# Kernel tuning notes

Measured on AMD Instinct MI355X. Metric: run time of the kernel, lower is better.

## Reference

```python
import jax, jax.numpy as jnp
import numpy as np

EMBED = 1024
HEADS = 16
HEAD_DIM = EMBED // HEADS
N, S = 2, 2048


def setup_inputs() -> dict:
    key = jax.random.key(0)
    ks = jax.random.split(key, 8)
    scale_p = 1.0 / np.sqrt(HEAD_DIM)
    return {
        "queries": jax.random.normal(ks[0], (N, S, EMBED), jnp.float32),
        "keys": jax.random.normal(ks[1], (N, S, EMBED), jnp.float32),
        "values": jax.random.normal(ks[2], (N, S, EMBED), jnp.float32),
        # per-head projection weights, torch Linear convention: y = x @ W.T
        "Wq": jax.random.normal(ks[3], (HEAD_DIM, HEAD_DIM), jnp.float32) * scale_p,
        "Wk": jax.random.normal(ks[4], (HEAD_DIM, HEAD_DIM), jnp.float32) * scale_p,
        "Wv": jax.random.normal(ks[5], (HEAD_DIM, HEAD_DIM), jnp.float32) * scale_p,
        "Wo": jax.random.normal(ks[6], (EMBED, EMBED), jnp.float32) * (1.0 / np.sqrt(EMBED)),
        "bo": jax.random.normal(ks[7], (EMBED,), jnp.float32) * 0.01,
    }


def reference(queries, keys, values, Wq, Wk, Wv, Wo, bo):
    n, sq, e = queries.shape
    sk = keys.shape[1]
    # split heads: (N, S, H, D)
    q = queries.reshape(n, sq, HEADS, HEAD_DIM)
    k = keys.reshape(n, sk, HEADS, HEAD_DIM)
    v = values.reshape(n, sk, HEADS, HEAD_DIM)
    # per-head linear projections (weights shared across heads), torch Linear: x @ W.T
    q = jnp.einsum('nshd,ed->nshe', q, Wq)
    k = jnp.einsum('nshd,ed->nshe', k, Wk)
    v = jnp.einsum('nshd,ed->nshe', v, Wv)
    # attention scores (N, H, Q, K); NOTE: scaled by sqrt(embed_size), as in source
    energy = jnp.einsum('nqhd,nkhd->nhqk', q, k)
    attention = jax.nn.softmax(energy / jnp.sqrt(jnp.float32(EMBED)), axis=3)
    out = jnp.einsum('nhql,nlhd->nqhd', attention, v).reshape(n, sq, EMBED)
    return out @ Wo.T + bo
```

## Files before the change

kernel.cpp:

```cpp
#include <hip/hip_runtime.h>
#include <hip/hip_bf16.h>

#define NB 2
#define SS 2048
#define EE 1024
#define HH 16
#define DD 64
#define NHD (NB*HH)
#define KT 64

#define QSCALE 0.04508422002777998f

typedef _Float16 half8 __attribute__((ext_vector_type(8)));
typedef _Float16 half4 __attribute__((ext_vector_type(4)));
typedef float floatx4 __attribute__((ext_vector_type(4)));

__device__ __forceinline__ half8 cvt8(const float* p) {
    float4 x = *(const float4*)p;
    float4 y = *(const float4*)(p + 4);
    half8 h = { (_Float16)x.x, (_Float16)x.y, (_Float16)x.z, (_Float16)x.w,
                (_Float16)y.x, (_Float16)y.y, (_Float16)y.z, (_Float16)y.w };
    return h;
}

__device__ __forceinline__ unsigned int pkrtz_u32(float a, float b) {
    return __builtin_bit_cast(unsigned int, __builtin_amdgcn_cvt_pkrtz(a, b));
}

__device__ __forceinline__ int swz64(int row, int colh) {
    return (row << 6) + ((((colh >> 3) ^ (row & 7)) << 3) | (colh & 7));
}

__global__ __launch_bounds__(256) void proj_kernel(
    const float* __restrict__ Q, const float* __restrict__ K, const float* __restrict__ V,
    const float* __restrict__ Wq, const float* __restrict__ Wk, const float* __restrict__ Wv,
    const float* __restrict__ Wo,
    _Float16* __restrict__ Qp, _Float16* __restrict__ Kp, _Float16* __restrict__ Vt,
    _Float16* __restrict__ Wf)
{
    int t = threadIdx.x, lane = t & 63, wid = t >> 6;
    int lr = lane & 15, lg = lane >> 4;
    int b = blockIdx.x;
    int nh = b >> 5, st = b & 31;
    int n = nh >> 4, h = nh & 15;

    if (t < 128) {
        int i = b * 1024 + t * 8;
        *(half8*)(Wf + i) = cvt8(Wo + i);
    }

    __shared__ __align__(16) _Float16 vt[DD][72];

    const size_t xoff = ((size_t)n * SS + st * 64 + wid * 16 + lr) * EE
                        + (size_t)h * DD + lg * 8;
    const size_t qob = ((size_t)nh * SS + st * 64 + wid * 16 + lg * 4) * DD;

    const float* tens[3] = {Q, K, V};
    const float* wts[3]  = {Wq, Wk, Wv};

    #pragma unroll
    for (int x = 0; x < 3; ++x) {
        const float* Xr = tens[x] + xoff;
        half8 a0 = cvt8(Xr);
        half8 a1 = cvt8(Xr + 32);
        floatx4 acc[4];
        #pragma unroll
        for (int ns = 0; ns < 4; ++ns) {
            const float* Wr = wts[x] + (size_t)(ns * 16 + lr) * DD + lg * 8;
            half8 b0 = cvt8(Wr);
            half8 b1 = cvt8(Wr + 32);
            floatx4 c = (floatx4){0.f, 0.f, 0.f, 0.f};
            c = __builtin_amdgcn_mfma_f32_16x16x32_f16(a0, b0, c, 0, 0, 0);
            c = __builtin_amdgcn_mfma_f32_16x16x32_f16(a1, b1, c, 0, 0, 0);
            acc[ns] = c;
        }
        if (x == 0) {
            #pragma unroll
            for (int ns = 0; ns < 4; ++ns)
                #pragma unroll
                for (int r = 0; r < 4; ++r)
                    Qp[qob + (size_t)r * DD + ns * 16 + lr] = (_Float16)(acc[ns][r] * QSCALE);
        } else if (x == 1) {
            #pragma unroll
            for (int ns = 0; ns < 4; ++ns)
                #pragma unroll
                for (int r = 0; r < 4; ++r)
                    Kp[qob + (size_t)r * DD + ns * 16 + lr] = (_Float16)acc[ns][r];
        } else {
            #pragma unroll
            for (int ns = 0; ns < 4; ++ns)
                #pragma unroll
                for (int r = 0; r < 4; ++r)
                    vt[ns * 16 + lr][wid * 16 + lg * 4 + r] = (_Float16)acc[ns][r];
        }
    }
    __syncthreads();
    {
        int d = t >> 2, q4 = (t & 3) * 16;
        _Float16* dst = Vt + ((size_t)nh * DD + d) * SS + st * 64 + q4;
        *(half8*)dst       = *(const half8*)(&vt[d][q4]);
        *(half8*)(dst + 8) = *(const half8*)(&vt[d][q4 + 8]);
    }
}

__global__ __launch_bounds__(256, 4) void attn_kernel(
    const _Float16* __restrict__ Qp, const _Float16* __restrict__ Kp,
    const _Float16* __restrict__ Vt, _Float16* __restrict__ Of)
{
    int b = blockIdx.x;
    int slot = b >> 3;
    int nh = (b & 7) * 4 + (slot & 3);
    int qt = slot >> 2;
    int n = nh >> 4, h = nh & 15;
    int t = threadIdx.x;
    int lane = t & 63, wid = t >> 6;
    int lr = lane & 15;
    int lg = lane >> 4;

    __shared__ __align__(16) _Float16 kbuf[2][KT * DD];
    __shared__ __align__(16) _Float16 vbuf[2][DD * KT];
    __shared__ __align__(16) _Float16 plds[4][16 * 64];

    const _Float16* Qb = Qp + ((size_t)nh * SS + qt * 64 + wid * 16) * DD;
    const _Float16* Kb = Kp + (size_t)nh * SS * DD;
    const _Float16* Vb = Vt + (size_t)nh * DD * SS;

    half8 qf0 = *(const half8*)(Qb + (size_t)lr * DD + lg * 8);
    half8 qf1 = *(const half8*)(Qb + (size_t)lr * DD + 32 + lg * 8);

    half8 ones = { (_Float16)1.f, (_Float16)1.f, (_Float16)1.f, (_Float16)1.f,
                   (_Float16)1.f, (_Float16)1.f, (_Float16)1.f, (_Float16)1.f };

    int sr = t >> 3, sc = (t & 7) * 8;

    {
        half8 k0 = *(const half8*)(Kb + (size_t)sr * DD + sc);
        half8 k1 = *(const half8*)(Kb + (size_t)(sr + 32) * DD + sc);
        half8 v0 = *(const half8*)(Vb + (size_t)sr * SS + sc);
        half8 v1 = *(const half8*)(Vb + (size_t)(sr + 32) * SS + sc);
        *(half8*)(&kbuf[0][swz64(sr, sc)]) = k0;
        *(half8*)(&kbuf[0][swz64(sr + 32, sc)]) = k1;
        *(half8*)(&vbuf[0][swz64(sr, sc)]) = v0;
        *(half8*)(&vbuf[0][swz64(sr + 32, sc)]) = v1;
    }
    __syncthreads();

    floatx4 oacc[4];
    #pragma unroll
    for (int ns = 0; ns < 4; ++ns) oacc[ns] = (floatx4){0.f, 0.f, 0.f, 0.f};
    floatx4 sacc = (floatx4){0.f, 0.f, 0.f, 0.f};

    int p = 0;
    for (int kb = 0; kb < SS; kb += KT, p ^= 1) {
        int kn = (kb + KT) & (SS - 1);
        half8 sk0 = *(const half8*)(Kb + (size_t)(kn + sr) * DD + sc);
        half8 sk1 = *(const half8*)(Kb + (size_t)(kn + sr + 32) * DD + sc);
        half8 sv0 = *(const half8*)(Vb + (size_t)sr * SS + kn + sc);
        half8 sv1 = *(const half8*)(Vb + (size_t)(sr + 32) * SS + kn + sc);

        half8 kf[4][2];
        #pragma unroll
        for (int ns = 0; ns < 4; ++ns) {
            kf[ns][0] = *(const half8*)(&kbuf[p][swz64(ns * 16 + lr, lg * 8)]);
            kf[ns][1] = *(const half8*)(&kbuf[p][swz64(ns * 16 + lr, 32 + lg * 8)]);
        }
        floatx4 s0 = (floatx4){0.f, 0.f, 0.f, 0.f};
        floatx4 s1 = (floatx4){0.f, 0.f, 0.f, 0.f};
        s0 = __builtin_amdgcn_mfma_f32_16x16x32_f16(kf[0][0], qf0, s0, 0, 0, 0);
        s0 = __builtin_amdgcn_mfma_f32_16x16x32_f16(kf[0][1], qf1, s0, 0, 0, 0);
        s1 = __builtin_amdgcn_mfma_f32_16x16x32_f16(kf[1][0], qf0, s1, 0, 0, 0);
        s1 = __builtin_amdgcn_mfma_f32_16x16x32_f16(kf[1][1], qf1, s1, 0, 0, 0);

        {
            float p0 = exp2f(fminf(s0[0], 50.f)), p1 = exp2f(fminf(s0[1], 50.f));
            float p2 = exp2f(fminf(s0[2], 50.f)), p3 = exp2f(fminf(s0[3], 50.f));
            uint2 pr; pr.x = pkrtz_u32(p0, p1); pr.y = pkrtz_u32(p2, p3);
            *(uint2*)(&plds[wid][swz64(lr, 0 * 16 + lg * 4)]) = pr;
        }
        {
            float p0 = exp2f(fminf(s1[0], 50.f)), p1 = exp2f(fminf(s1[1], 50.f));
            float p2 = exp2f(fminf(s1[2], 50.f)), p3 = exp2f(fminf(s1[3], 50.f));
            uint2 pr; pr.x = pkrtz_u32(p0, p1); pr.y = pkrtz_u32(p2, p3);
            *(uint2*)(&plds[wid][swz64(lr, 1 * 16 + lg * 4)]) = pr;
        }

        floatx4 s2 = (floatx4){0.f, 0.f, 0.f, 0.f};
        floatx4 s3 = (floatx4){0.f, 0.f, 0.f, 0.f};
        s2 = __builtin_amdgcn_mfma_f32_16x16x32_f16(kf[2][0], qf0, s2, 0, 0, 0);
        s2 = __builtin_amdgcn_mfma_f32_16x16x32_f16(kf[2][1], qf1, s2, 0, 0, 0);
        s3 = __builtin_amdgcn_mfma_f32_16x16x32_f16(kf[3][0], qf0, s3, 0, 0, 0);
        s3 = __builtin_amdgcn_mfma_f32_16x16x32_f16(kf[3][1], qf1, s3, 0, 0, 0);

        half8 vf[4][2];
        #pragma unroll
        for (int ns = 0; ns < 4; ++ns) {
            vf[ns][0] = *(const half8*)(&vbuf[p][swz64(ns * 16 + lr, lg * 8)]);
            vf[ns][1] = *(const half8*)(&vbuf[p][swz64(ns * 16 + lr, 32 + lg * 8)]);
        }

        asm volatile("s_waitcnt lgkmcnt(0)" ::: "memory");
        half8 pf0 = *(const half8*)(&plds[wid][swz64(lr, lg * 8)]);

        {
            float p0 = exp2f(fminf(s2[0], 50.f)), p1 = exp2f(fminf(s2[1], 50.f));
            float p2 = exp2f(fminf(s2[2], 50.f)), p3 = exp2f(fminf(s2[3], 50.f));
            uint2 pr; pr.x = pkrtz_u32(p0, p1); pr.y = pkrtz_u32(p2, p3);
            *(uint2*)(&plds[wid][swz64(lr, 2 * 16 + lg * 4)]) = pr;
        }
        {
            float p0 = exp2f(fminf(s3[0], 50.f)), p1 = exp2f(fminf(s3[1], 50.f));
            float p2 = exp2f(fminf(s3[2], 50.f)), p3 = exp2f(fminf(s3[3], 50.f));
            uint2 pr; pr.x = pkrtz_u32(p0, p1); pr.y = pkrtz_u32(p2, p3);
            *(uint2*)(&plds[wid][swz64(lr, 3 * 16 + lg * 4)]) = pr;
        }

        #pragma unroll
        for (int ns = 0; ns < 4; ++ns)
            oacc[ns] = __builtin_amdgcn_mfma_f32_16x16x32_f16(pf0, vf[ns][0], oacc[ns], 0, 0, 0);
        sacc = __builtin_amdgcn_mfma_f32_16x16x32_f16(pf0, ones, sacc, 0, 0, 0);

        asm volatile("s_waitcnt lgkmcnt(0)" ::: "memory");
        half8 pf1 = *(const half8*)(&plds[wid][swz64(lr, 32 + lg * 8)]);

        #pragma unroll
        for (int ns = 0; ns < 4; ++ns)
            oacc[ns] = __builtin_amdgcn_mfma_f32_16x16x32_f16(pf1, vf[ns][1], oacc[ns], 0, 0, 0);
        sacc = __builtin_amdgcn_mfma_f32_16x16x32_f16(pf1, ones, sacc, 0, 0, 0);

        *(half8*)(&kbuf[p ^ 1][swz64(sr, sc)]) = sk0;
        *(half8*)(&kbuf[p ^ 1][swz64(sr + 32, sc)]) = sk1;
        *(half8*)(&vbuf[p ^ 1][swz64(sr, sc)]) = sv0;
        *(half8*)(&vbuf[p ^ 1][swz64(sr + 32, sc)]) = sv1;
        __syncthreads();
    }

    float linv[4];
    #pragma unroll
    for (int r = 0; r < 4; ++r)
        linv[r] = 1.f / sacc[r];

    _Float16* Ob = Of + ((size_t)n * SS + qt * 64 + wid * 16) * EE + h * DD;
    #pragma unroll
    for (int ns = 0; ns < 4; ++ns)
        #pragma unroll
        for (int r = 0; r < 4; ++r)
            Ob[(size_t)(lg * 4 + r) * EE + ns * 16 + lr] = (_Float16)(oacc[ns][r] * linv[r]);
}

__global__ __launch_bounds__(256, 2) void oproj_kernel(
    const _Float16* __restrict__ Of, const _Float16* __restrict__ Wf,
    const float* __restrict__ bo, float* __restrict__ out)
{
    int b = blockIdx.x;
    int mb = b & 63, nb = b >> 6;
    int t = threadIdx.x, lane = t & 63, wid = t >> 6;
    int wm = wid >> 1, wn = wid & 1;
    int lr = lane & 15, lg = lane >> 4;
    int m0 = mb * 64, n0 = nb * 128;

    __shared__ __align__(16) _Float16 As[2][64][72];
    __shared__ __align__(16) _Float16 Bs[2][128][72];

    int arow = t >> 2, acol = (t & 3) * 16;
    int brow = t >> 1, bcol = (t & 1) * 32;
    const _Float16* Ag = Of + (size_t)(m0 + arow) * EE + acol;
    const _Float16* Bg = Wf + (size_t)(n0 + brow) * EE + bcol;

    floatx4 acc[2][4];
    #pragma unroll
    for (int sm = 0; sm < 2; ++sm)
        #pragma unroll
        for (int sn = 0; sn < 4; ++sn) acc[sm][sn] = (floatx4){0.f, 0.f, 0.f, 0.f};

    #pragma unroll
    for (int j = 0; j < 2; ++j)
        *(half8*)(&As[0][arow][acol + j * 8]) = *(const half8*)(Ag + j * 8);
    #pragma unroll
    for (int j = 0; j < 4; ++j)
        *(half8*)(&Bs[0][brow][bcol + j * 8]) = *(const half8*)(Bg + j * 8);
    __syncthreads();

    int p = 0;
    for (int kb = 0; kb < EE; kb += 64, p ^= 1) {
        int kn = kb + 64;
        half8 sa[2], sb[4];
        if (kn < EE) {
            #pragma unroll
            for (int j = 0; j < 2; ++j) sa[j] = *(const half8*)(Ag + kn + j * 8);
            #pragma unroll
            for (int j = 0; j < 4; ++j) sb[j] = *(const half8*)(Bg + kn + j * 8);
        }
        #pragma unroll
        for (int kk = 0; kk < 2; ++kk) {
            half8 af[2], bf[4];
            #pragma unroll
            for (int s = 0; s < 2; ++s)
                af[s] = *(const half8*)(&As[p][wm * 32 + s * 16 + lr][kk * 32 + lg * 8]);
            #pragma unroll
            for (int s = 0; s < 4; ++s)
                bf[s] = *(const half8*)(&Bs[p][wn * 64 + s * 16 + lr][kk * 32 + lg * 8]);
            #pragma unroll
            for (int sm = 0; sm < 2; ++sm)
                #pragma unroll
                for (int sn = 0; sn < 4; ++sn)
                    acc[sm][sn] = __builtin_amdgcn_mfma_f32_16x16x32_f16(
                        af[sm], bf[sn], acc[sm][sn], 0, 0, 0);
        }
        if (kn < EE) {
            #pragma unroll
            for (int j = 0; j < 2; ++j)
                *(half8*)(&As[p ^ 1][arow][acol + j * 8]) = sa[j];
            #pragma unroll
            for (int j = 0; j < 4; ++j)
                *(half8*)(&Bs[p ^ 1][brow][bcol + j * 8]) = sb[j];
        }
        __syncthreads();
    }

    #pragma unroll
    for (int sn = 0; sn < 4; ++sn) {
        int nn = n0 + wn * 64 + sn * 16 + lr;
        float bn = bo[nn];
        #pragma unroll
        for (int sm = 0; sm < 2; ++sm) {
            #pragma unroll
            for (int r = 0; r < 4; ++r)
                out[(size_t)(m0 + wm * 32 + sm * 16 + lg * 4 + r) * EE + nn]
                    = acc[sm][sn][r] + bn;
        }
    }
}

extern "C" void kernel_launch(void* const* d_in, const int* in_sizes, int n_in,
                              void* d_out, int out_size, void* d_ws, size_t ws_size,
                              hipStream_t stream)
{
    const float* Q  = (const float*)d_in[0];
    const float* K  = (const float*)d_in[1];
    const float* V  = (const float*)d_in[2];
    const float* Wq = (const float*)d_in[3];
    const float* Wk = (const float*)d_in[4];
    const float* Wv = (const float*)d_in[5];
    const float* Wo = (const float*)d_in[6];
    const float* bo = (const float*)d_in[7];
    float* out = (float*)d_out;

    const size_t NSE = (size_t)NB * SS * EE;
    _Float16* Qp = (_Float16*)d_ws;
    _Float16* Kp = Qp + NSE;
    _Float16* Vt = Kp + NSE;
    _Float16* Of = Vt + NSE;
    _Float16* Wf = Of + NSE;

    proj_kernel<<<1024, 256, 0, stream>>>(Q, K, V, Wq, Wk, Wv, Wo, Qp, Kp, Vt, Wf);
    attn_kernel<<<NHD * (SS / 64), 256, 0, stream>>>(Qp, Kp, Vt, Of);
    oproj_kernel<<<512, 256, 0, stream>>>(Of, Wf, bo, out);
}
```

Measured before the change: 206.0 us.

## Switch attention to 32x32x16 MFMA with 128-row query tiles and register P

Rewrites the attention inner loop to use 32x32x16 MFMA tiles, so each wave handles 32 query rows and each block 128. The softmax probabilities now go into the PV MFMA operand through v_permlane32_swap in registers instead of a round trip through LDS. This halves the block count and doubles K/V reuse per block, cutting LDS traffic and the waitcnt stalls. In exchange, register pressure rises (occupancy hint lowered to 2) and there are fewer blocks to spread across the CUs.

```diff
diff --git a/kernel.cpp b/kernel.cpp
--- a/kernel.cpp
+++ b/kernel.cpp
@@ -12,8 +12,8 @@
 #define QSCALE 0.04508422002777998f
 
 typedef _Float16 half8 __attribute__((ext_vector_type(8)));
-typedef _Float16 half4 __attribute__((ext_vector_type(4)));
 typedef float floatx4 __attribute__((ext_vector_type(4)));
+typedef float floatx16 __attribute__((ext_vector_type(16)));
 
 __device__ __forceinline__ half8 cvt8(const float* p) {
     float4 x = *(const float4*)p;
@@ -103,7 +103,7 @@
     }
 }
 
-__global__ __launch_bounds__(256, 4) void attn_kernel(
+__global__ __launch_bounds__(256, 2) void attn_kernel(
     const _Float16* __restrict__ Qp, const _Float16* __restrict__ Kp,
     const _Float16* __restrict__ Vt, _Float16* __restrict__ Of)
 {
@@ -114,19 +114,19 @@
     int n = nh >> 4, h = nh & 15;
     int t = threadIdx.x;
     int lane = t & 63, wid = t >> 6;
-    int lr = lane & 15;
-    int lg = lane >> 4;
+    int l31 = lane & 31, h5 = lane >> 5;
 
     __shared__ __align__(16) _Float16 kbuf[2][KT * DD];
     __shared__ __align__(16) _Float16 vbuf[2][DD * KT];
-    __shared__ __align__(16) _Float16 plds[4][16 * 64];
-
-    const _Float16* Qb = Qp + ((size_t)nh * SS + qt * 64 + wid * 16) * DD;
+
     const _Float16* Kb = Kp + (size_t)nh * SS * DD;
     const _Float16* Vb = Vt + (size_t)nh * DD * SS;
 
-    half8 qf0 = *(const half8*)(Qb + (size_t)lr * DD + lg * 8);
-    half8 qf1 = *(const half8*)(Qb + (size_t)lr * DD + 32 + lg * 8);
+    const _Float16* Qb = Qp + ((size_t)nh * SS + qt * 128 + wid * 32 + l31) * DD;
+    half8 qf[4];
+    #pragma unroll
+    for (int c = 0; c < 4; ++c)
+        qf[c] = *(const half8*)(Qb + c * 16 + h5 * 8);
 
     half8 ones = { (_Float16)1.f, (_Float16)1.f, (_Float16)1.f, (_Float16)1.f,
                    (_Float16)1.f, (_Float16)1.f, (_Float16)1.f, (_Float16)1.f };
@@ -145,10 +145,8 @@
     }
     __syncthreads();
 
-    floatx4 oacc[4];
-    #pragma unroll
-    for (int ns = 0; ns < 4; ++ns) oacc[ns] = (floatx4){0.f, 0.f, 0.f, 0.f};
-    floatx4 sacc = (floatx4){0.f, 0.f, 0.f, 0.f};
+    floatx16 oacc0 = {}, oacc1 = {};
+    floatx16 sacc  = {};
 
     int p = 0;
     for (int kb = 0; kb < SS; kb += KT, p ^= 1) {
@@ -158,74 +156,58 @@
         half8 sv0 = *(const half8*)(Vb + (size_t)sr * SS + kn + sc);
         half8 sv1 = *(const half8*)(Vb + (size_t)(sr + 32) * SS + kn + sc);
 
-        half8 kf[4][2];
-        #pragma unroll
-        for (int ns = 0; ns < 4; ++ns) {
-            kf[ns][0] = *(const half8*)(&kbuf[p][swz64(ns * 16 + lr, lg * 8)]);
-            kf[ns][1] = *(const half8*)(&kbuf[p][swz64(ns * 16 + lr, 32 + lg * 8)]);
-        }
-        floatx4 s0 = (floatx4){0.f, 0.f, 0.f, 0.f};
-        floatx4 s1 = (floatx4){0.f, 0.f, 0.f, 0.f};
-        s0 = __builtin_amdgcn_mfma_f32_16x16x32_f16(kf[0][0], qf0, s0, 0, 0, 0);
-        s0 = __builtin_amdgcn_mfma_f32_16x16x32_f16(kf[0][1], qf1, s0, 0, 0, 0);
-        s1 = __builtin_amdgcn_mfma_f32_16x16x32_f16(kf[1][0], qf0, s1, 0, 0, 0);
-        s1 = __builtin_amdgcn_mfma_f32_16x16x32_f16(kf[1][1], qf1, s1, 0, 0, 0);
-
-        {
-            float p0 = exp2f(fminf(s0[0], 50.f)), p1 = exp2f(fminf(s0[1], 50.f));
-            float p2 = exp2f(fminf(s0[2], 50.f)), p3 = exp2f(fminf(s0[3], 50.f));
-            uint2 pr; pr.x = pkrtz_u32(p0, p1); pr.y = pkrtz_u32(p2, p3);
-            *(uint2*)(&plds[wid][swz64(lr, 0 * 16 + lg * 4)]) = pr;
-        }
-        {
-            float p0 = exp2f(fminf(s1[0], 50.f)), p1 = exp2f(fminf(s1[1], 50.f));
-            float p2 = exp2f(fminf(s1[2], 50.f)), p3 = exp2f(fminf(s1[3], 50.f));
-            uint2 pr; pr.x = pkrtz_u32(p0, p1); pr.y = pkrtz_u32(p2, p3);
-            *(uint2*)(&plds[wid][swz64(lr, 1 * 16 + lg * 4)]) = pr;
-        }
-
-        floatx4 s2 = (floatx4){0.f, 0.f, 0.f, 0.f};
-        floatx4 s3 = (floatx4){0.f, 0.f, 0.f, 0.f};
-        s2 = __builtin_amdgcn_mfma_f32_16x16x32_f16(kf[2][0], qf0, s2, 0, 0, 0);
-        s2 = __builtin_amdgcn_mfma_f32_16x16x32_f16(kf[2][1], qf1, s2, 0, 0, 0);
-        s3 = __builtin_amdgcn_mfma_f32_16x16x32_f16(kf[3][0], qf0, s3, 0, 0, 0);
-        s3 = __builtin_amdgcn_mfma_f32_16x16x32_f16(kf[3][1], qf1, s3, 0, 0, 0);
-
-        half8 vf[4][2];
-        #pragma unroll
-        for (int ns = 0; ns < 4; ++ns) {
-            vf[ns][0] = *(const half8*)(&vbuf[p][swz64(ns * 16 + lr, lg * 8)]);
-            vf[ns][1] = *(const half8*)(&vbuf[p][swz64(ns * 16 + lr, 32 + lg * 8)]);
-        }
-
-        asm volatile("s_waitcnt lgkmcnt(0)" ::: "memory");
-        half8 pf0 = *(const half8*)(&plds[wid][swz64(lr, lg * 8)]);
-
-        {
-            float p0 = exp2f(fminf(s2[0], 50.f)), p1 = exp2f(fminf(s2[1], 50.f));
-            float p2 = exp2f(fminf(s2[2], 50.f)), p3 = exp2f(fminf(s2[3], 50.f));
-            uint2 pr; pr.x = pkrtz_u32(p0, p1); pr.y = pkrtz_u32(p2, p3);
-            *(uint2*)(&plds[wid][swz64(lr, 2 * 16 + lg * 4)]) = pr;
-        }
-        {
-            float p0 = exp2f(fminf(s3[0], 50.f)), p1 = exp2f(fminf(s3[1], 50.f));
-            float p2 = exp2f(fminf(s3[2], 50.f)), p3 = exp2f(fminf(s3[3], 50.f));
-            uint2 pr; pr.x = pkrtz_u32(p0, p1); pr.y = pkrtz_u32(p2, p3);
-            *(uint2*)(&plds[wid][swz64(lr, 3 * 16 + lg * 4)]) = pr;
-        }
-
-        #pragma unroll
-        for (int ns = 0; ns < 4; ++ns)
-            oacc[ns] = __builtin_amdgcn_mfma_f32_16x16x32_f16(pf0, vf[ns][0], oacc[ns], 0, 0, 0);
-        sacc = __builtin_amdgcn_mfma_f32_16x16x32_f16(pf0, ones, sacc, 0, 0, 0);
-
-        asm volatile("s_waitcnt lgkmcnt(0)" ::: "memory");
-        half8 pf1 = *(const half8*)(&plds[wid][swz64(lr, 32 + lg * 8)]);
-
-        #pragma unroll
-        for (int ns = 0; ns < 4; ++ns)
-            oacc[ns] = __builtin_amdgcn_mfma_f32_16x16x32_f16(pf1, vf[ns][1], oacc[ns], 0, 0, 0);
-        sacc = __builtin_amdgcn_mfma_f32_16x16x32_f16(pf1, ones, sacc, 0, 0, 0);
+        floatx16 s0 = {}, s1 = {};
+        #pragma unroll
+        for (int c = 0; c < 4; ++c) {
+            half8 kf0 = *(const half8*)(&kbuf[p][swz64(l31,      c * 16 + h5 * 8)]);
+            half8 kf1 = *(const half8*)(&kbuf[p][swz64(32 + l31, c * 16 + h5 * 8)]);
+            s0 = __builtin_amdgcn_mfma_f32_32x32x16_f16(kf0, qf[c], s0, 0, 0, 0);
+            s1 = __builtin_amdgcn_mfma_f32_32x32x16_f16(kf1, qf[c], s1, 0, 0, 0);
+        }
+
+        half8 pf[4];
+        #pragma unroll
+        for (int kt2 = 0; kt2 < 2; ++kt2) {
+            const floatx16& sv = kt2 ? s1 : s0;
+            unsigned int w0, w1, w2, w3, w4, w5, w6, w7;
+            {
+                float e0 = exp2f(fminf(sv[0], 50.f)), e1 = exp2f(fminf(sv[1], 50.f));
+                float e2 = exp2f(fminf(sv[2], 50.f)), e3 = exp2f(fminf(sv[3], 50.f));
+                w0 = pkrtz_u32(e0, e1); w1 = pkrtz_u32(e2, e3);
+            }
+            {
+                float e0 = exp2f(fminf(sv[4], 50.f)), e1 = exp2f(fminf(sv[5], 50.f));
+                float e2 = exp2f(fminf(sv[6], 50.f)), e3 = exp2f(fminf(sv[7], 50.f));
+                w2 = pkrtz_u32(e0, e1); w3 = pkrtz_u32(e2, e3);
+            }
+            {
+                float e0 = exp2f(fminf(sv[8], 50.f)), e1 = exp2f(fminf(sv[9], 50.f));
+                float e2 = exp2f(fminf(sv[10], 50.f)), e3 = exp2f(fminf(sv[11], 50.f));
+                w4 = pkrtz_u32(e0, e1); w5 = pkrtz_u32(e2, e3);
+            }
+            {
+                float e0 = exp2f(fminf(sv[12], 50.f)), e1 = exp2f(fminf(sv[13], 50.f));
+                float e2 = exp2f(fminf(sv[14], 50.f)), e3 = exp2f(fminf(sv[15], 50.f));
+                w6 = pkrtz_u32(e0, e1); w7 = pkrtz_u32(e2, e3);
+            }
+            asm("v_permlane32_swap_b32 %0, %1" : "+v"(w0), "+v"(w2));
+            asm("v_permlane32_swap_b32 %0, %1" : "+v"(w1), "+v"(w3));
+            asm("v_permlane32_swap_b32 %0, %1" : "+v"(w4), "+v"(w6));
+            asm("v_permlane32_swap_b32 %0, %1" : "+v"(w5), "+v"(w7));
+            uint4 ua = {w0, w1, w2, w3};
+            uint4 ub = {w4, w5, w6, w7};
+            pf[kt2 * 2 + 0] = __builtin_bit_cast(half8, ua);
+            pf[kt2 * 2 + 1] = __builtin_bit_cast(half8, ub);
+        }
+
+        #pragma unroll
+        for (int c = 0; c < 4; ++c) {
+            half8 vf0 = *(const half8*)(&vbuf[p][swz64(l31,      c * 16 + h5 * 8)]);
+            half8 vf1 = *(const half8*)(&vbuf[p][swz64(32 + l31, c * 16 + h5 * 8)]);
+            oacc0 = __builtin_amdgcn_mfma_f32_32x32x16_f16(pf[c], vf0, oacc0, 0, 0, 0);
+            oacc1 = __builtin_amdgcn_mfma_f32_32x32x16_f16(pf[c], vf1, oacc1, 0, 0, 0);
+            sacc  = __builtin_amdgcn_mfma_f32_32x32x16_f16(pf[c], ones, sacc, 0, 0, 0);
+        }
 
         *(half8*)(&kbuf[p ^ 1][swz64(sr, sc)]) = sk0;
         *(half8*)(&kbuf[p ^ 1][swz64(sr + 32, sc)]) = sk1;
@@ -234,17 +216,14 @@
         __syncthreads();
     }
 
-    float linv[4];
-    #pragma unroll
-    for (int r = 0; r < 4; ++r)
-        linv[r] = 1.f / sacc[r];
-
-    _Float16* Ob = Of + ((size_t)n * SS + qt * 64 + wid * 16) * EE + h * DD;
-    #pragma unroll
-    for (int ns = 0; ns < 4; ++ns)
-        #pragma unroll
-        for (int r = 0; r < 4; ++r)
-            Ob[(size_t)(lg * 4 + r) * EE + ns * 16 + lr] = (_Float16)(oacc[ns][r] * linv[r]);
+    _Float16* Ob = Of + ((size_t)n * SS + qt * 128 + wid * 32) * EE + h * DD;
+    #pragma unroll
+    for (int r = 0; r < 16; ++r) {
+        float linv = 1.f / sacc[r];
+        int qrow = (r & 3) + 8 * (r >> 2) + 4 * h5;
+        Ob[(size_t)qrow * EE + l31]      = (_Float16)(oacc0[r] * linv);
+        Ob[(size_t)qrow * EE + 32 + l31] = (_Float16)(oacc1[r] * linv);
+    }
 }
 
 __global__ __launch_bounds__(256, 2) void oproj_kernel(
@@ -353,6 +332,6 @@
     _Float16* Wf = Of + NSE;
 
     proj_kernel<<<1024, 256, 0, stream>>>(Q, K, V, Wq, Wk, Wv, Wo, Qp, Kp, Vt, Wf);
-    attn_kernel<<<NHD * (SS / 64), 256, 0, stream>>>(Qp, Kp, Vt, Of);
+    attn_kernel<<<512, 256, 0, stream>>>(Qp, Kp, Vt, Of);
     oproj_kernel<<<512, 256, 0, stream>>>(Of, Wf, bo, out);
 }
```

Result: no change. 203.5 us (-1.2%).
